# Optimization experiments

Hardware: AMD Instinct MI355X
Metric: run time of the kernel (lower is better)

The kernel has to match this reference:

```python
import jax, jax.numpy as jnp
import numpy as np

B, S, H, D = 4, 2048, 16, 128
E = H * D  # emb_dim = 2048


def setup_inputs() -> dict:
    key = jax.random.key(0)
    ks = jax.random.split(key, 9)
    s_in = 1.0 / np.sqrt(E)
    return {
        "inputs": jax.random.normal(ks[0], (B, S, E), dtype=jnp.float32),
        "Wq": jax.random.normal(ks[1], (E, E), dtype=jnp.float32) * s_in,
        "bq": jnp.zeros((E,), dtype=jnp.float32),
        "Wk": jax.random.normal(ks[2], (E, E), dtype=jnp.float32) * s_in,
        "bk": jnp.zeros((E,), dtype=jnp.float32),
        "Wv": jax.random.normal(ks[3], (E, E), dtype=jnp.float32) * s_in,
        "bv": jnp.zeros((E,), dtype=jnp.float32),
        "Wo": jax.random.normal(ks[4], (E, E), dtype=jnp.float32) * s_in,
        "bo": jnp.zeros((E,), dtype=jnp.float32),
    }


def reference(inputs, Wq, bq, Wk, bk, Wv, bv, Wo, bo):
    b, s, e = inputs.shape
    # QKV projections -> [B, H, S, D]
    q = (inputs @ Wq + bq).reshape(b, s, H, D).transpose(0, 2, 1, 3)
    k = (inputs @ Wk + bk).reshape(b, s, H, D).transpose(0, 2, 1, 3)
    v = (inputs @ Wv + bv).reshape(b, s, H, D).transpose(0, 2, 1, 3)
    scale = 1.0 / jnp.sqrt(jnp.asarray(D, dtype=q.dtype))
    # Scaled dot-product attention (what the blockwise flash loop computes)
    scores = jnp.einsum('bhqd,bhkd->bhqk', q, k) * scale
    probs = jax.nn.softmax(scores, axis=-1)
    attn = jnp.einsum('bhqk,bhkd->bhqd', probs, v)
    attn = attn.transpose(0, 2, 1, 3).reshape(b, s, e)
    return attn @ Wo + bo
```

## Files before the change

kernel.cpp:

```cpp
#include <hip/hip_runtime.h>
#include <hip/hip_bf16.h>
#include <stdint.h>

typedef __bf16 bf16;
typedef float f32x4 __attribute__((ext_vector_type(4)));
typedef bf16 bf16x4 __attribute__((ext_vector_type(4)));
typedef bf16 bf16x8 __attribute__((ext_vector_type(8)));

#define DEV __device__ __forceinline__

DEV void gload16(const void* g, void* l) {
  __builtin_amdgcn_global_load_lds((const __attribute__((address_space(1))) void*)g,
                                   (__attribute__((address_space(3))) void*)l, 16, 0, 0);
}

DEV f32x4 mfma16(bf16x8 a, bf16x8 b, f32x4 c) {
  return __builtin_amdgcn_mfma_f32_16x16x32_bf16(a, b, c, 0, 0, 0);
}

#if __has_builtin(__builtin_amdgcn_exp2f)
DEV float EXP2F(float x) { return __builtin_amdgcn_exp2f(x); }
#else
DEV float EXP2F(float x) { return exp2f(x); }
#endif

static constexpr int Bn = 4, Sn = 2048, Hn = 16, Dn = 128, En = 2048, Mn = 8192;

__global__ void cvt_x(const float* __restrict__ in, bf16* __restrict__ out, int n8) {
  int i = blockIdx.x * blockDim.x + threadIdx.x;
  int stride = gridDim.x * blockDim.x;
  for (int idx = i; idx < n8; idx += stride) {
    const float4* p = (const float4*)(in + (size_t)idx * 8);
    float4 a = p[0], b = p[1];
    bf16x8 o;
    o[0]=(bf16)a.x; o[1]=(bf16)a.y; o[2]=(bf16)a.z; o[3]=(bf16)a.w;
    o[4]=(bf16)b.x; o[5]=(bf16)b.y; o[6]=(bf16)b.z; o[7]=(bf16)b.w;
    *(bf16x8*)(out + (size_t)idx * 8) = o;
  }
}

__global__ void wtrans(const float* __restrict__ W, bf16* __restrict__ Wt) {
  __shared__ bf16 t[64][65];
  int tx = threadIdx.x & 15, ty = threadIdx.x >> 4;
  int c0 = blockIdx.x * 64, r0 = blockIdx.y * 64;
  #pragma unroll
  for (int i = 0; i < 4; ++i) {
    int r = i * 16 + ty;
    float4 v = *(const float4*)&W[(size_t)(r0 + r) * En + c0 + tx * 4];
    t[r][tx*4+0] = (bf16)v.x; t[r][tx*4+1] = (bf16)v.y;
    t[r][tx*4+2] = (bf16)v.z; t[r][tx*4+3] = (bf16)v.w;
  }
  __syncthreads();
  #pragma unroll
  for (int i = 0; i < 4; ++i) {
    int c = i * 16 + ty;
    bf16x4 o;
    #pragma unroll
    for (int j = 0; j < 4; ++j) o[j] = t[tx*4+j][c];
    *(bf16x4*)&Wt[(size_t)(c0 + c) * En + r0 + tx * 4] = o;
  }
}

__global__ void vtrans(const bf16* __restrict__ V, bf16* __restrict__ Vt) {
  __shared__ bf16 t[64][65];
  int tx = threadIdx.x & 15, ty = threadIdx.x >> 4;
  int s0 = blockIdx.x * 64, d0 = blockIdx.y * 64, bh = blockIdx.z;
  const bf16* Vi = V + (size_t)bh * Sn * Dn;
  bf16* Vo = Vt + (size_t)bh * Sn * Dn;
  #pragma unroll
  for (int i = 0; i < 4; ++i) {
    int r = i * 16 + ty;
    bf16x4 v = *(const bf16x4*)&Vi[(size_t)(s0 + r) * Dn + d0 + tx * 4];
    #pragma unroll
    for (int j = 0; j < 4; ++j) t[r][tx*4+j] = v[j];
  }
  __syncthreads();
  #pragma unroll
  for (int i = 0; i < 4; ++i) {
    int dd = i * 16 + ty;
    bf16x4 o;
    #pragma unroll
    for (int j = 0; j < 4; ++j) o[j] = t[tx*4+j][dd];
    *(bf16x4*)&Vo[(size_t)(d0 + dd) * Sn + s0 + tx * 4] = o;
  }
}

#define STAGE_A(H, DBUF, KTN) do { \
    const bf16* s_ = A + (size_t)(mbase + (tid >> 2)) * K + (KTN) * 64 + (H) * 32 \
                     + (((tid & 3) ^ ((tid >> 3) & 3)) * 8); \
    uint8_t* d_ = (DBUF) + (H) * 16384 + (w << 10); \
    gload16(s_, d_); \
    gload16(s_ + (size_t)128 * K, d_ + 8192); \
  } while (0)
#define STAGE_B(H, DBUF, KTN) do { \
    const bf16* s_ = Bt + (size_t)(nbase + (tid >> 2)) * K + (KTN) * 64 + (H) * 32 \
                     + (((tid & 3) ^ ((tid >> 3) & 3)) * 8); \
    uint8_t* d_ = (DBUF) + (H) * 16384 + (w << 10); \
    gload16(s_, d_); \
    gload16(s_ + (size_t)128 * K, d_ + 8192); \
  } while (0)

template<int OUT_MODE>
__global__ __launch_bounds__(512, 2) void gemm256(
    const bf16* __restrict__ A, const bf16* __restrict__ Bt,
    const float* __restrict__ b0, const float* __restrict__ b1,
    const float* __restrict__ b2, void* __restrict__ Cout,
    int M, int N, int K, int nbx)
{
  __shared__ __align__(16) uint8_t smem[131072];
  const int tid = threadIdx.x, lane = tid & 63, w = tid >> 6;
  const int wm = w >> 2, wn = w & 3;
  const int g = lane >> 4, lr = lane & 15;
  const int gx = (g ^ ((lr >> 1) & 3)) << 4;
  const int lid = blockIdx.x;
  const int swz = (lid & 7) * ((int)gridDim.x >> 3) + (lid >> 3);
  const int bx = swz % nbx, by = swz / nbx;
  const int mbase = by * 256, nbase = bx * 256;

  f32x4 acc[8][4] = {};

  STAGE_A(0, smem, 0);
  STAGE_B(0, smem + 65536, 0);
  STAGE_A(1, smem, 0);
  STAGE_B(1, smem + 65536, 0);
  asm volatile("s_waitcnt vmcnt(4)" ::: "memory");
  __builtin_amdgcn_s_barrier();

  const int NKT = K >> 6;
  for (int kt = 0; kt < NKT; ++kt) {
    const int cur = kt & 1;
    uint8_t* Acur = smem + (cur << 15);
    uint8_t* Bcur = smem + 65536 + (cur << 15);
    uint8_t* Anxt = smem + ((cur ^ 1) << 15);
    uint8_t* Bnxt = smem + 65536 + ((cur ^ 1) << 15);
    const bool notlast = (kt + 1 < NKT);
    bf16x8 af[8], bfr0, bfr1;

    #pragma unroll
    for (int mf = 0; mf < 8; ++mf)
      af[mf] = *(const bf16x8*)(Acur + (wm * 128 + mf * 16 + lr) * 64 + gx);
    bfr0 = *(const bf16x8*)(Bcur + (wn * 64 +  0 + lr) * 64 + gx);
    bfr1 = *(const bf16x8*)(Bcur + (wn * 64 + 16 + lr) * 64 + gx);
    if (notlast) STAGE_A(0, Anxt, kt + 1);
    __builtin_amdgcn_s_barrier();
    asm volatile("s_waitcnt lgkmcnt(0)" ::: "memory");
    __builtin_amdgcn_sched_barrier(0);
    __builtin_amdgcn_s_setprio(1);
    #pragma unroll
    for (int mf = 0; mf < 8; ++mf) {
      acc[mf][0] = mfma16(af[mf], bfr0, acc[mf][0]);
      acc[mf][1] = mfma16(af[mf], bfr1, acc[mf][1]);
    }
    __builtin_amdgcn_s_setprio(0);
    __builtin_amdgcn_s_barrier();

    bfr0 = *(const bf16x8*)(Bcur + (wn * 64 + 32 + lr) * 64 + gx);
    bfr1 = *(const bf16x8*)(Bcur + (wn * 64 + 48 + lr) * 64 + gx);
    if (notlast) STAGE_B(0, Bnxt, kt + 1);
    __builtin_amdgcn_s_barrier();
    asm volatile("s_waitcnt lgkmcnt(0)" ::: "memory");
    __builtin_amdgcn_sched_barrier(0);
    __builtin_amdgcn_s_setprio(1);
    #pragma unroll
    for (int mf = 0; mf < 8; ++mf) {
      acc[mf][2] = mfma16(af[mf], bfr0, acc[mf][2]);
      acc[mf][3] = mfma16(af[mf], bfr1, acc[mf][3]);
    }
    __builtin_amdgcn_s_setprio(0);
    if (notlast) { asm volatile("s_waitcnt vmcnt(4)" ::: "memory"); }
    else         { asm volatile("s_waitcnt vmcnt(0)" ::: "memory"); }
    __builtin_amdgcn_s_barrier();

    #pragma unroll
    for (int mf = 0; mf < 8; ++mf)
      af[mf] = *(const bf16x8*)(Acur + 16384 + (wm * 128 + mf * 16 + lr) * 64 + gx);
    bfr0 = *(const bf16x8*)(Bcur + 16384 + (wn * 64 +  0 + lr) * 64 + gx);
    bfr1 = *(const bf16x8*)(Bcur + 16384 + (wn * 64 + 16 + lr) * 64 + gx);
    if (notlast) STAGE_A(1, Anxt, kt + 1);
    __builtin_amdgcn_s_barrier();
    asm volatile("s_waitcnt lgkmcnt(0)" ::: "memory");
    __builtin_amdgcn_sched_barrier(0);
    __builtin_amdgcn_s_setprio(1);
    #pragma unroll
    for (int mf = 0; mf < 8; ++mf) {
      acc[mf][0] = mfma16(af[mf], bfr0, acc[mf][0]);
      acc[mf][1] = mfma16(af[mf], bfr1, acc[mf][1]);
    }
    __builtin_amdgcn_s_setprio(0);
    __builtin_amdgcn_s_barrier();

    bfr0 = *(const bf16x8*)(Bcur + 16384 + (wn * 64 + 32 + lr) * 64 + gx);
    bfr1 = *(const bf16x8*)(Bcur + 16384 + (wn * 64 + 48 + lr) * 64 + gx);
    if (notlast) STAGE_B(1, Bnxt, kt + 1);
    __builtin_amdgcn_s_barrier();
    asm volatile("s_waitcnt lgkmcnt(0)" ::: "memory");
    __builtin_amdgcn_sched_barrier(0);
    __builtin_amdgcn_s_setprio(1);
    #pragma unroll
    for (int mf = 0; mf < 8; ++mf) {
      acc[mf][2] = mfma16(af[mf], bfr0, acc[mf][2]);
      acc[mf][3] = mfma16(af[mf], bfr1, acc[mf][3]);
    }
    __builtin_amdgcn_s_setprio(0);
    asm volatile("s_waitcnt vmcnt(4)" ::: "memory");
    __builtin_amdgcn_s_barrier();
  }

  int tsel = 0;
  const float* bsel = b0;
  if constexpr (OUT_MODE == 0) {
    tsel = nbase >> 11;
    bsel = (tsel == 0) ? b0 : ((tsel == 1) ? b1 : b2);
  }
  #pragma unroll
  for (int j = 0; j < 4; ++j) {
    int n = nbase + wn * 64 + j * 16 + lr;
    float bv = (OUT_MODE == 0) ? bsel[n & 2047] : bsel[n];
    #pragma unroll
    for (int mf = 0; mf < 8; ++mf) {
      #pragma unroll
      for (int r = 0; r < 4; ++r) {
        int m = mbase + wm * 128 + mf * 16 + g * 4 + r;
        float val = acc[mf][j][r] + bv;
        if constexpr (OUT_MODE == 0) {
          int b = m >> 11, s = m & 2047, nn = n & 2047, h = nn >> 7, d = nn & 127;
          ((bf16*)Cout)[(size_t)tsel * ((size_t)Mn * En) +
                        ((size_t)(b * Hn + h) * Sn + s) * Dn + d] = (bf16)val;
        } else {
          ((float*)Cout)[(size_t)m * N + n] = val;
        }
      }
    }
  }
}

__global__ __launch_bounds__(256, 2) void attn(
    const bf16* __restrict__ Q, const bf16* __restrict__ K,
    const bf16* __restrict__ Vt, bf16* __restrict__ O)
{
  __shared__ __align__(16) uint8_t smem[65536];
  const int tid = threadIdx.x, lane = tid & 63, w = tid >> 6;
  const int g = lane >> 4, lr = lane & 15;
  const int lid = blockIdx.x + (int)gridDim.x * blockIdx.y;
  const int xcd = lid & 7, j = lid >> 3;
  const int bh = xcd * 8 + (j >> 4);
  const int q0 = (j & 15) * 128;
  const size_t hoff = (size_t)bh * Sn * Dn;
  const bf16* Qh = Q + hoff;
  const bf16* Kh = K + hoff;
  const bf16* Vh = Vt + hoff;
  const float SC2 = 0.12751744f;

  #pragma unroll
  for (int it = 0; it < 8; ++it) {
    int cl = it * 256 + tid;
    int row = cl >> 4, cs = cl & 15;
    int cg = cs ^ (row & 7);
    gload16(Qh + (size_t)(q0 + row) * Dn + cg * 8, smem + (it * 256 + (tid & ~63)) * 16);
  }
  __syncthreads();
  bf16x8 qf[2][4];
  #pragma unroll
  for (int nf = 0; nf < 2; ++nf)
    #pragma unroll
    for (int ks = 0; ks < 4; ++ks) {
      int row = w * 32 + nf * 16 + lr;
      qf[nf][ks] = *(const bf16x8*)(smem + row * 256 + (((ks * 4 + g) ^ (row & 7)) << 4));
    }
  __syncthreads();

  const int vd = tid >> 1, vhw = tid & 1;
  const bf16* vrow = Vh + (size_t)vd * Sn + vhw * 32;

  uint4 vr0, vr1, vr2, vr3;
  #pragma unroll
  for (int it = 0; it < 4; ++it) {
    int cl = it * 256 + tid;
    int row = cl >> 4, cs = cl & 15;
    int cg = cs ^ (row & 7);
    gload16(Kh + (size_t)row * Dn + cg * 8, smem + (it * 256 + (tid & ~63)) * 16);
  }
  { const uint4* vs = (const uint4*)vrow;
    vr0 = vs[0]; vr1 = vs[1]; vr2 = vs[2]; vr3 = vs[3]; }

  f32x4 o[2][8] = {};
  float m2[2] = { -__builtin_inff(), -__builtin_inff() };
  float lrun[2] = { 0.f, 0.f };

  for (int t = 0; t < 32; ++t) {
    const int cur = t & 1;
    uint8_t* Kcur = smem + (cur << 14);
    uint8_t* Knxt = smem + ((cur ^ 1) << 14);
    uint8_t* Vcur = smem + 32768 + (cur << 14);
    asm volatile("s_waitcnt vmcnt(0)" ::: "memory");
    {
      uint8_t* base = Vcur + vd * 128;
      const int sw = vd & 7, cb = vhw * 4;
      *(uint4*)(base + (((cb + 0) ^ sw) << 4)) = make_uint4(vr0.x, vr0.y, vr2.x, vr2.y);
      *(uint4*)(base + (((cb + 1) ^ sw) << 4)) = make_uint4(vr0.z, vr0.w, vr2.z, vr2.w);
      *(uint4*)(base + (((cb + 2) ^ sw) << 4)) = make_uint4(vr1.x, vr1.y, vr3.x, vr3.y);
      *(uint4*)(base + (((cb + 3) ^ sw) << 4)) = make_uint4(vr1.z, vr1.w, vr3.z, vr3.w);
    }
    if (t < 31) {
      const int kvn = (t + 1) * 64;
      #pragma unroll
      for (int it = 0; it < 4; ++it) {
        int cl = it * 256 + tid;
        int row = cl >> 4, cs = cl & 15;
        int cg = cs ^ (row & 7);
        gload16(Kh + (size_t)(kvn + row) * Dn + cg * 8,
                Knxt + (it * 256 + (tid & ~63)) * 16);
      }
      const uint4* vs = (const uint4*)(vrow + kvn);
      vr0 = vs[0]; vr1 = vs[1]; vr2 = vs[2]; vr3 = vs[3];
    }
    asm volatile("s_waitcnt lgkmcnt(0)" ::: "memory");
    asm volatile("s_barrier" ::: "memory");

    f32x4 sfr[2][4] = {};
    __builtin_amdgcn_s_setprio(1);
    #pragma unroll
    for (int ks = 0; ks < 4; ++ks) {
      #pragma unroll
      for (int mf = 0; mf < 4; ++mf) {
        int row = mf * 16 + lr;
        bf16x8 kf = *(const bf16x8*)(Kcur + row * 256 + (((ks * 4 + g) ^ (row & 7)) << 4));
        sfr[0][mf] = mfma16(kf, qf[0][ks], sfr[0][mf]);
        sfr[1][mf] = mfma16(kf, qf[1][ks], sfr[1][mf]);
      }
    }
    __builtin_amdgcn_s_setprio(0);

    bf16x8 pa[2][2];
    #pragma unroll
    for (int nf = 0; nf < 2; ++nf) {
      f32x4 a0, a1;
      #pragma unroll
      for (int r = 0; r < 4; ++r) a0[r] = fmaxf(sfr[nf][0][r], sfr[nf][1][r]);
      #pragma unroll
      for (int r = 0; r < 4; ++r) a1[r] = fmaxf(sfr[nf][2][r], sfr[nf][3][r]);
      #pragma unroll
      for (int r = 0; r < 4; ++r) a0[r] = fmaxf(a0[r], a1[r]);
      float mx = fmaxf(fmaxf(a0[0], a0[1]), fmaxf(a0[2], a0[3]));
      mx = fmaxf(mx, __shfl_xor(mx, 16));
      mx = fmaxf(mx, __shfl_xor(mx, 32));
      float pm2 = mx * SC2;
      if (__any(pm2 > m2[nf] + 8.f)) {
        float mnew = fmaxf(m2[nf], pm2);
        float fsc = EXP2F(m2[nf] - mnew);
        m2[nf] = mnew;
        lrun[nf] *= fsc;
        float fv[4];
        #pragma unroll
        for (int r = 0; r < 4; ++r) fv[r] = __shfl(fsc, g * 4 + r);
        #pragma unroll
        for (int df = 0; df < 8; ++df)
          #pragma unroll
          for (int r = 0; r < 4; ++r) o[nf][df][r] *= fv[r];
      }
      const float mc = m2[nf];
      f32x4 p[4];
      #pragma unroll
      for (int mf = 0; mf < 4; ++mf)
        #pragma unroll
        for (int r = 0; r < 4; ++r)
          p[mf][r] = EXP2F(__builtin_fmaf(sfr[nf][mf][r], SC2, -mc));
      f32x4 s0, s1;
      #pragma unroll
      for (int r = 0; r < 4; ++r) s0[r] = p[0][r] + p[1][r];
      #pragma unroll
      for (int r = 0; r < 4; ++r) s1[r] = p[2][r] + p[3][r];
      #pragma unroll
      for (int r = 0; r < 4; ++r) s0[r] += s1[r];
      float ps = (s0[0] + s0[1]) + (s0[2] + s0[3]);
      ps += __shfl_xor(ps, 16);
      ps += __shfl_xor(ps, 32);
      lrun[nf] += ps;
      #pragma unroll
      for (int ks = 0; ks < 2; ++ks) {
        bf16x8 tt;
        #pragma unroll
        for (int i = 0; i < 4; ++i) {
          tt[i]     = (bf16)p[2 * ks][i];
          tt[i + 4] = (bf16)p[2 * ks + 1][i];
        }
        pa[nf][ks] = tt;
      }
    }

    __builtin_amdgcn_s_setprio(1);
    #pragma unroll
    for (int ks = 0; ks < 2; ++ks) {
      #pragma unroll
      for (int df = 0; df < 8; ++df) {
        int row = df * 16 + lr;
        bf16x8 vf = *(const bf16x8*)(Vcur + row * 128 + (((ks * 4 + g) ^ (row & 7)) << 4));
        o[0][df] = mfma16(pa[0][ks], vf, o[0][df]);
        o[1][df] = mfma16(pa[1][ks], vf, o[1][df]);
      }
    }
    __builtin_amdgcn_s_setprio(0);
    asm volatile("s_barrier" ::: "memory");
  }

  const int b = bh >> 4, h = bh & 15;
  #pragma unroll
  for (int nf = 0; nf < 2; ++nf) {
    float inv = 1.f / lrun[nf];
    float iv[4];
    #pragma unroll
    for (int r = 0; r < 4; ++r) iv[r] = __shfl(inv, g * 4 + r);
    #pragma unroll
    for (int df = 0; df < 8; ++df) {
      #pragma unroll
      for (int r = 0; r < 4; ++r) {
        int qrow = q0 + w * 32 + nf * 16 + g * 4 + r;
        int d = df * 16 + lr;
        size_t m = (size_t)b * Sn + qrow;
        O[m * En + h * Dn + d] = (bf16)(o[nf][df][r] * iv[r]);
      }
    }
  }
}

extern "C" void kernel_launch(void* const* d_in, const int* in_sizes, int n_in,
                              void* d_out, int out_size, void* d_ws, size_t ws_size,
                              hipStream_t stream) {
  const float* X  = (const float*)d_in[0];
  const float* Wq = (const float*)d_in[1];
  const float* bq = (const float*)d_in[2];
  const float* Wk = (const float*)d_in[3];
  const float* bk = (const float*)d_in[4];
  const float* Wv = (const float*)d_in[5];
  const float* bv = (const float*)d_in[6];
  const float* Wo = (const float*)d_in[7];
  const float* bo = (const float*)d_in[8];

  bf16* ws = (bf16*)d_ws;
  const size_t szE = (size_t)Mn * En;
  const size_t szW = (size_t)En * En;
  bf16* Xb  = ws;
  bf16* Wqt = Xb + szE;
  bf16* Wkt = Wqt + szW;
  bf16* Wvt = Wkt + szW;
  bf16* Wot = Wvt + szW;
  bf16* Qb  = Wot + szW;
  bf16* Kb  = Qb + szE;
  bf16* Vb  = Kb + szE;
  bf16* Vtp = Vb + szE;
  bf16* AO  = Vb;

  cvt_x<<<2048, 256, 0, stream>>>(X, Xb, (int)(szE / 8));
  wtrans<<<dim3(32, 32), 256, 0, stream>>>(Wq, Wqt);
  wtrans<<<dim3(32, 32), 256, 0, stream>>>(Wk, Wkt);
  wtrans<<<dim3(32, 32), 256, 0, stream>>>(Wv, Wvt);
  wtrans<<<dim3(32, 32), 256, 0, stream>>>(Wo, Wot);
  gemm256<0><<<768, 512, 0, stream>>>(Xb, Wqt, bq, bk, bv, Qb, Mn, 3 * En, En, 24);
  vtrans<<<dim3(32, 2, 64), 256, 0, stream>>>(Vb, Vtp);
  attn<<<dim3(16, 64), 256, 0, stream>>>(Qb, Kb, Vtp, AO);
  gemm256<1><<<256, 512, 0, stream>>>(AO, Wot, bo, nullptr, nullptr, d_out, Mn, En, En, 8);
}
```

Before: 493.6 us.

## Fuse V transpose into QKV GEMM epilogue and enlarge attention blocks

The QKV GEMM epilogue now writes V directly in transposed [B,H,D,S] layout with 4-wide bf16 stores, which removes the separate vtrans kernel and its extra read and write of V. The attention kernel moves to 512-thread blocks covering 256 query rows (8 waves), so each K/V tile staged in shared memory serves twice as many queries and per-thread K/V load work halves. The launch bounds change to (512,4), which tightens register limits and may cause spills. The transposed V stores are strided across S, so they may coalesce less well.

After: 645.8 us. 1.31x slower.

```diff
diff --git a/kernel.cpp b/kernel.cpp
--- a/kernel.cpp
+++ b/kernel.cpp
@@ -58,30 +58,6 @@
     #pragma unroll
     for (int j = 0; j < 4; ++j) o[j] = t[tx*4+j][c];
     *(bf16x4*)&Wt[(size_t)(c0 + c) * En + r0 + tx * 4] = o;
-  }
-}
-
-__global__ void vtrans(const bf16* __restrict__ V, bf16* __restrict__ Vt) {
-  __shared__ bf16 t[64][65];
-  int tx = threadIdx.x & 15, ty = threadIdx.x >> 4;
-  int s0 = blockIdx.x * 64, d0 = blockIdx.y * 64, bh = blockIdx.z;
-  const bf16* Vi = V + (size_t)bh * Sn * Dn;
-  bf16* Vo = Vt + (size_t)bh * Sn * Dn;
-  #pragma unroll
-  for (int i = 0; i < 4; ++i) {
-    int r = i * 16 + ty;
-    bf16x4 v = *(const bf16x4*)&Vi[(size_t)(s0 + r) * Dn + d0 + tx * 4];
-    #pragma unroll
-    for (int j = 0; j < 4; ++j) t[r][tx*4+j] = v[j];
-  }
-  __syncthreads();
-  #pragma unroll
-  for (int i = 0; i < 4; ++i) {
-    int dd = i * 16 + ty;
-    bf16x4 o;
-    #pragma unroll
-    for (int j = 0; j < 4; ++j) o[j] = t[tx*4+j][dd];
-    *(bf16x4*)&Vo[(size_t)(d0 + dd) * Sn + s0 + tx * 4] = o;
   }
 }
 
@@ -105,6 +81,7 @@
     const bf16* __restrict__ A, const bf16* __restrict__ Bt,
     const float* __restrict__ b0, const float* __restrict__ b1,
     const float* __restrict__ b2, void* __restrict__ Cout,
+    bf16* __restrict__ Vout,
     int M, int N, int K, int nbx)
 {
   __shared__ __align__(16) uint8_t smem[131072];
@@ -206,45 +183,72 @@
     __builtin_amdgcn_s_barrier();
   }
 
-  int tsel = 0;
-  const float* bsel = b0;
   if constexpr (OUT_MODE == 0) {
-    tsel = nbase >> 11;
-    bsel = (tsel == 0) ? b0 : ((tsel == 1) ? b1 : b2);
-  }
-  #pragma unroll
-  for (int j = 0; j < 4; ++j) {
-    int n = nbase + wn * 64 + j * 16 + lr;
-    float bv = (OUT_MODE == 0) ? bsel[n & 2047] : bsel[n];
-    #pragma unroll
-    for (int mf = 0; mf < 8; ++mf) {
-      #pragma unroll
-      for (int r = 0; r < 4; ++r) {
-        int m = mbase + wm * 128 + mf * 16 + g * 4 + r;
-        float val = acc[mf][j][r] + bv;
-        if constexpr (OUT_MODE == 0) {
-          int b = m >> 11, s = m & 2047, nn = n & 2047, h = nn >> 7, d = nn & 127;
-          ((bf16*)Cout)[(size_t)tsel * ((size_t)Mn * En) +
-                        ((size_t)(b * Hn + h) * Sn + s) * Dn + d] = (bf16)val;
-        } else {
-          ((float*)Cout)[(size_t)m * N + n] = val;
+    int tsel = nbase >> 11;
+    if (tsel == 2) {
+      #pragma unroll
+      for (int j = 0; j < 4; ++j) {
+        int nn = (nbase + wn * 64 + j * 16 + lr) & 2047;
+        int h = nn >> 7, d = nn & 127;
+        float bv = b2[nn];
+        #pragma unroll
+        for (int mf = 0; mf < 8; ++mf) {
+          int m0 = mbase + wm * 128 + mf * 16 + g * 4;
+          int b = m0 >> 11, s0 = m0 & 2047;
+          bf16x4 o4;
+          #pragma unroll
+          for (int r = 0; r < 4; ++r) o4[r] = (bf16)(acc[mf][j][r] + bv);
+          *(bf16x4*)&Vout[((size_t)(b * Hn + h) * Dn + d) * Sn + s0] = o4;
         }
       }
-    }
-  }
-}
-
-__global__ __launch_bounds__(256, 2) void attn(
+    } else {
+      const float* bsel = (tsel == 0) ? b0 : b1;
+      #pragma unroll
+      for (int j = 0; j < 4; ++j) {
+        int n = nbase + wn * 64 + j * 16 + lr;
+        int nn = n & 2047;
+        float bv = bsel[nn];
+        int h = nn >> 7, d = nn & 127;
+        #pragma unroll
+        for (int mf = 0; mf < 8; ++mf) {
+          #pragma unroll
+          for (int r = 0; r < 4; ++r) {
+            int m = mbase + wm * 128 + mf * 16 + g * 4 + r;
+            int b = m >> 11, s = m & 2047;
+            ((bf16*)Cout)[(size_t)tsel * ((size_t)Mn * En) +
+                          ((size_t)(b * Hn + h) * Sn + s) * Dn + d] = (bf16)(acc[mf][j][r] + bv);
+          }
+        }
+      }
+    }
+  } else {
+    #pragma unroll
+    for (int j = 0; j < 4; ++j) {
+      int n = nbase + wn * 64 + j * 16 + lr;
+      float bv = b0[n];
+      #pragma unroll
+      for (int mf = 0; mf < 8; ++mf) {
+        #pragma unroll
+        for (int r = 0; r < 4; ++r) {
+          int m = mbase + wm * 128 + mf * 16 + g * 4 + r;
+          ((float*)Cout)[(size_t)m * N + n] = acc[mf][j][r] + bv;
+        }
+      }
+    }
+  }
+}
+
+__global__ __launch_bounds__(512, 4) void attn(
     const bf16* __restrict__ Q, const bf16* __restrict__ K,
     const bf16* __restrict__ Vt, bf16* __restrict__ O)
 {
   __shared__ __align__(16) uint8_t smem[65536];
   const int tid = threadIdx.x, lane = tid & 63, w = tid >> 6;
   const int g = lane >> 4, lr = lane & 15;
-  const int lid = blockIdx.x + (int)gridDim.x * blockIdx.y;
+  const int lid = blockIdx.x;
   const int xcd = lid & 7, j = lid >> 3;
-  const int bh = xcd * 8 + (j >> 4);
-  const int q0 = (j & 15) * 128;
+  const int bh = xcd * 8 + (j >> 3);
+  const int q0 = (j & 7) * 256;
   const size_t hoff = (size_t)bh * Sn * Dn;
   const bf16* Qh = Q + hoff;
   const bf16* Kh = K + hoff;
@@ -253,10 +257,10 @@
 
   #pragma unroll
   for (int it = 0; it < 8; ++it) {
-    int cl = it * 256 + tid;
+    int cl = it * 512 + tid;
     int row = cl >> 4, cs = cl & 15;
     int cg = cs ^ (row & 7);
-    gload16(Qh + (size_t)(q0 + row) * Dn + cg * 8, smem + (it * 256 + (tid & ~63)) * 16);
+    gload16(Qh + (size_t)(q0 + row) * Dn + cg * 8, smem + (it * 512 + (tid & ~63)) * 16);
   }
   __syncthreads();
   bf16x8 qf[2][4];
@@ -269,19 +273,18 @@
     }
   __syncthreads();
 
-  const int vd = tid >> 1, vhw = tid & 1;
-  const bf16* vrow = Vh + (size_t)vd * Sn + vhw * 32;
-
-  uint4 vr0, vr1, vr2, vr3;
-  #pragma unroll
-  for (int it = 0; it < 4; ++it) {
-    int cl = it * 256 + tid;
+  const int vd = tid >> 2, vq = tid & 3;
+  const bf16* vrow = Vh + (size_t)vd * Sn + (vq >> 1) * 32 + (vq & 1) * 8;
+
+  uint4 u0, u1;
+  #pragma unroll
+  for (int it = 0; it < 2; ++it) {
+    int cl = it * 512 + tid;
     int row = cl >> 4, cs = cl & 15;
     int cg = cs ^ (row & 7);
-    gload16(Kh + (size_t)row * Dn + cg * 8, smem + (it * 256 + (tid & ~63)) * 16);
-  }
-  { const uint4* vs = (const uint4*)vrow;
-    vr0 = vs[0]; vr1 = vs[1]; vr2 = vs[2]; vr3 = vs[3]; }
+    gload16(Kh + (size_t)row * Dn + cg * 8, smem + (it * 512 + (tid & ~63)) * 16);
+  }
+  { const uint4* vs = (const uint4*)vrow; u0 = vs[0]; u1 = vs[2]; }
 
   f32x4 o[2][8] = {};
   float m2[2] = { -__builtin_inff(), -__builtin_inff() };
@@ -295,24 +298,22 @@
     asm volatile("s_waitcnt vmcnt(0)" ::: "memory");
     {
       uint8_t* base = Vcur + vd * 128;
-      const int sw = vd & 7, cb = vhw * 4;
-      *(uint4*)(base + (((cb + 0) ^ sw) << 4)) = make_uint4(vr0.x, vr0.y, vr2.x, vr2.y);
-      *(uint4*)(base + (((cb + 1) ^ sw) << 4)) = make_uint4(vr0.z, vr0.w, vr2.z, vr2.w);
-      *(uint4*)(base + (((cb + 2) ^ sw) << 4)) = make_uint4(vr1.x, vr1.y, vr3.x, vr3.y);
-      *(uint4*)(base + (((cb + 3) ^ sw) << 4)) = make_uint4(vr1.z, vr1.w, vr3.z, vr3.w);
+      const int sw = vd & 7;
+      *(uint4*)(base + (((2 * vq + 0) ^ sw) << 4)) = make_uint4(u0.x, u0.y, u1.x, u1.y);
+      *(uint4*)(base + (((2 * vq + 1) ^ sw) << 4)) = make_uint4(u0.z, u0.w, u1.z, u1.w);
     }
     if (t < 31) {
       const int kvn = (t + 1) * 64;
       #pragma unroll
-      for (int it = 0; it < 4; ++it) {
-        int cl = it * 256 + tid;
+      for (int it = 0; it < 2; ++it) {
+        int cl = it * 512 + tid;
         int row = cl >> 4, cs = cl & 15;
         int cg = cs ^ (row & 7);
         gload16(Kh + (size_t)(kvn + row) * Dn + cg * 8,
-                Knxt + (it * 256 + (tid & ~63)) * 16);
+                Knxt + (it * 512 + (tid & ~63)) * 16);
       }
       const uint4* vs = (const uint4*)(vrow + kvn);
-      vr0 = vs[0]; vr1 = vs[1]; vr2 = vs[2]; vr3 = vs[3];
+      u0 = vs[0]; u1 = vs[2];
     }
     asm volatile("s_waitcnt lgkmcnt(0)" ::: "memory");
     asm volatile("s_barrier" ::: "memory");
@@ -455,8 +456,7 @@
   wtrans<<<dim3(32, 32), 256, 0, stream>>>(Wk, Wkt);
   wtrans<<<dim3(32, 32), 256, 0, stream>>>(Wv, Wvt);
   wtrans<<<dim3(32, 32), 256, 0, stream>>>(Wo, Wot);
-  gemm256<0><<<768, 512, 0, stream>>>(Xb, Wqt, bq, bk, bv, Qb, Mn, 3 * En, En, 24);
-  vtrans<<<dim3(32, 2, 64), 256, 0, stream>>>(Vb, Vtp);
-  attn<<<dim3(16, 64), 256, 0, stream>>>(Qb, Kb, Vtp, AO);
-  gemm256<1><<<256, 512, 0, stream>>>(AO, Wot, bo, nullptr, nullptr, d_out, Mn, En, En, 8);
-}
+  gemm256<0><<<768, 512, 0, stream>>>(Xb, Wqt, bq, bk, bv, Qb, Vtp, Mn, 3 * En, En, 24);
+  attn<<<512, 512, 0, stream>>>(Qb, Kb, Vtp, AO);
+  gemm256<1><<<256, 512, 0, stream>>>(AO, Wot, bo, nullptr, nullptr, d_out, nullptr, Mn, En, En, 8);
+}
```
